# Performance work log

Measured on AMD Instinct MI355X. Metric: run time of the kernel, lower is better.

The kernel has to match this reference:

```python
import jax, jax.numpy as jnp
import numpy as np

B, DIN, D, T, C = 32768, 784, 256, 16, 64


def setup_inputs() -> dict:
    key = jax.random.key(0)
    ks = jax.random.split(key, 4)
    x = jax.random.normal(ks[0], (B, DIN), dtype=jnp.float32)
    Wp = jax.random.normal(ks[1], (DIN, D), dtype=jnp.float32) / np.sqrt(DIN).astype(np.float32)
    bp = jnp.zeros((D,), jnp.float32)
    sigs_raw = jax.random.normal(ks[2], (T, D), dtype=jnp.float32) * 0.5
    Wc = jax.random.normal(ks[3], (T, D, C), dtype=jnp.float32) / np.sqrt(D).astype(np.float32)
    bc = jnp.zeros((T, C), jnp.float32)
    return {"x": x, "Wp": Wp, "bp": bp, "sigs_raw": sigs_raw, "Wc": Wc, "bc": bc}


def _quantize_ternary(s):
    # straight-through ternary quantization with +/-0.3 thresholds
    q = jnp.where(s > 0.3, 1.0, jnp.where(s < -0.3, -1.0, 0.0)).astype(s.dtype)
    return s + jax.lax.stop_gradient(q - s)


def reference(x, Wp, bp, sigs_raw, Wc, bc):
    h = x @ Wp + bp                                   # [B, D]
    sigs = _quantize_ternary(sigs_raw)                # [T, D] ternary signatures
    scores = h @ sigs.T                               # [B, T]
    tile_indices = jnp.argmax(scores, axis=-1)        # [B] top-1 routing
    # per-tile linear classifiers, then select the routed tile's logits
    all_logits = jnp.einsum('bd,tdc->btc', h, Wc) + bc[None]   # [B, T, C]
    logits = jnp.take_along_axis(all_logits, tile_indices[:, None, None], axis=1)[:, 0, :]
    return logits, tile_indices
```

## Files before the change

kernel.cpp:

```cpp
#include <hip/hip_runtime.h>

typedef short short8 __attribute__((ext_vector_type(8)));
typedef float f32x4 __attribute__((ext_vector_type(4)));

#define B_ROWS 32768
#define DIN 784
#define D_DIM 256
#define T_TILES 16
#define C_DIM 64
#define BM 128
#define NCHUNK 25

#define WPT_OFF    0u
#define WCT_OFF    409600u
#define WS_OFF     933888u
#define BS_OFF     1034240u
#define H_OFF      1034368u
#define BUCKET_OFF 17811584u
#define CNT_OFF    19908736u

static __device__ inline unsigned short f2bf(float f) {
    unsigned u = __builtin_bit_cast(unsigned, f);
    u += 0x7fffu + ((u >> 16) & 1u);
    return (unsigned short)(u >> 16);
}
static __device__ inline double qtern(float s) {
    double v = (double)s;
    return (v > 0.3) ? 1.0 : ((v < -0.3) ? -1.0 : 0.0);
}

__global__ __launch_bounds__(256)
void prep_kernel(const float* __restrict__ Wp, const float* __restrict__ bp,
                 const float* __restrict__ sigs_raw, const float* __restrict__ Wc,
                 char* __restrict__ ws) {
    const int bid = blockIdx.x, tid = threadIdx.x;
    unsigned short* wpt = (unsigned short*)(ws + WPT_OFF);
    unsigned short* wct = (unsigned short*)(ws + WCT_OFF);
    double* Wsd = (double*)(ws + WS_OFF);
    double* bsd = (double*)(ws + BS_OFF);

    if (bid < 800) {
        const int k = bid;
        const float v = (k < DIN) ? Wp[(size_t)k * D_DIM + tid] : 0.f;
        wpt[(k >> 5) * 8192 + tid * 32 + (k & 31)] = f2bf(v);
    } else if (bid < 1584) {
        const int k = bid - 800;
        const int t = tid >> 4, l = tid & 15;
        double s = 0.0;
        for (int j = 0; j < 16; ++j) {
            const int d = l + 16 * j;
            s += (double)Wp[(size_t)k * D_DIM + d] * qtern(sigs_raw[t * D_DIM + d]);
        }
        #pragma unroll
        for (int m = 8; m >= 1; m >>= 1) s += __shfl_xor(s, m);
        if (l == 0) Wsd[k * 16 + t] = s;
    } else if (bid < 1600) {
        const int t = bid - 1584;
        const int c4 = (tid & 15) * 4, dg = (tid >> 4) * 16;
        for (int j = 0; j < 16; ++j) {
            const int d = dg + j;
            const float4 v = *(const float4*)&Wc[((size_t)t * D_DIM + d) * C_DIM + c4];
            wct[t * 16384 + (c4 + 0) * 256 + d] = f2bf(v.x);
            wct[t * 16384 + (c4 + 1) * 256 + d] = f2bf(v.y);
            wct[t * 16384 + (c4 + 2) * 256 + d] = f2bf(v.z);
            wct[t * 16384 + (c4 + 3) * 256 + d] = f2bf(v.w);
        }
    } else {
        if (tid < 16) {
            double s = 0.0;
            for (int d = 0; d < D_DIM; ++d)
                s += (double)bp[d] * qtern(sigs_raw[tid * D_DIM + d]);
            bsd[tid] = s;
        }
    }
}

__global__ __launch_bounds__(256, 2)
void gemm_score_kernel(const float* __restrict__ x, const float* __restrict__ bp,
                       char* __restrict__ ws, float* __restrict__ out) {
    __shared__ __align__(16) char u[61440];
    __shared__ int tidx_s[BM];

    unsigned short* Abuf = (unsigned short*)u;
    unsigned short* Bbuf = (unsigned short*)(u + 20480);
    const unsigned short* wpt = (const unsigned short*)(ws + WPT_OFF);
    unsigned short* hbf = (unsigned short*)(ws + H_OFF);
    const double* Wsd = (const double*)(ws + WS_OFF);
    const double* bsd = (const double*)(ws + BS_OFF);
    int* bucket = (int*)(ws + BUCKET_OFF);
    int* cnt = (int*)(ws + CNT_OFF);

    const int tid = threadIdx.x;
    const int row0 = blockIdx.x * BM;
    const int wid = tid >> 6, lane = tid & 63;
    const int wr = wid >> 1, wcid = wid & 1;
    const int lrow = lane & 15, kb8 = (lane >> 4) * 8;
    const int ar = tid >> 1, ako = (tid & 1) * 16;

    f32x4 acc[4][8];
    #pragma unroll
    for (int i = 0; i < 4; ++i)
        #pragma unroll
        for (int j = 0; j < 8; ++j) acc[i][j] = (f32x4){0.f, 0.f, 0.f, 0.f};

    float4 va[4], vb[4];
    {
        const bool valid = ako < DIN;
        const float4* p = (const float4*)&x[(size_t)(row0 + ar) * DIN + ako];
        va[0] = p[0]; va[1] = p[1]; va[2] = p[2]; va[3] = p[3];
        (void)valid;
        const float4* q = (const float4*)(wpt + 0 * 8192 + tid * 32);
        vb[0] = q[0]; vb[1] = q[1]; vb[2] = q[2]; vb[3] = q[3];
        unsigned short tmp[16];
        const float* f = (const float*)va;
        #pragma unroll
        for (int i = 0; i < 16; ++i) tmp[i] = f2bf(f[i]);
        unsigned short* da = Abuf + ar * 40 + ako;
        *(short8*)da = *(short8*)tmp; *(short8*)(da + 8) = *(short8*)(tmp + 8);
        unsigned short* db = Bbuf + tid * 40;
        *(float4*)db = vb[0]; *(float4*)(db + 8) = vb[1];
        *(float4*)(db + 16) = vb[2]; *(float4*)(db + 24) = vb[3];
    }
    __syncthreads();

    for (int c = 0; c < NCHUNK; ++c) {
        const int cur = c & 1;
        if (c + 1 < NCHUNK) {
            const int kbase = (c + 1) * 32 + ako;
            if (kbase < DIN) {
                const float4* p = (const float4*)&x[(size_t)(row0 + ar) * DIN + kbase];
                va[0] = p[0]; va[1] = p[1]; va[2] = p[2]; va[3] = p[3];
            } else {
                va[0] = va[1] = va[2] = va[3] = make_float4(0, 0, 0, 0);
            }
            const float4* q = (const float4*)(wpt + (c + 1) * 8192 + tid * 32);
            vb[0] = q[0]; vb[1] = q[1]; vb[2] = q[2]; vb[3] = q[3];
        }
        {
            const unsigned short* Ab = Abuf + cur * 5120;
            const unsigned short* Bb = Bbuf + cur * 10240;
            short8 af[4];
            #pragma unroll
            for (int rf = 0; rf < 4; ++rf)
                af[rf] = *(const short8*)(Ab + (wr * 64 + rf * 16 + lrow) * 40 + kb8);
            #pragma unroll
            for (int cf = 0; cf < 8; ++cf) {
                const short8 bfr = *(const short8*)(Bb + (wcid * 128 + cf * 16 + lrow) * 40 + kb8);
                #pragma unroll
                for (int rf = 0; rf < 4; ++rf)
                    acc[rf][cf] = __builtin_amdgcn_mfma_f32_16x16x32_bf16(af[rf], bfr, acc[rf][cf], 0, 0, 0);
            }
        }
        if (c + 1 < NCHUNK) {
            unsigned short tmp[16];
            const float* f = (const float*)va;
            #pragma unroll
            for (int i = 0; i < 16; ++i) tmp[i] = f2bf(f[i]);
            unsigned short* da = Abuf + (cur ^ 1) * 5120 + ar * 40 + ako;
            *(short8*)da = *(short8*)tmp; *(short8*)(da + 8) = *(short8*)(tmp + 8);
            unsigned short* db = Bbuf + (cur ^ 1) * 10240 + tid * 40;
            *(float4*)db = vb[0]; *(float4*)(db + 8) = vb[1];
            *(float4*)(db + 16) = vb[2]; *(float4*)(db + 24) = vb[3];
        }
        __syncthreads();
    }

    #pragma unroll
    for (int cf = 0; cf < 8; ++cf) {
        const int gc = wcid * 128 + cf * 16 + lrow;
        const float bpv = bp[gc];
        #pragma unroll
        for (int rf = 0; rf < 4; ++rf) {
            const int grow = row0 + wr * 64 + rf * 16 + (lane >> 4) * 4;
            #pragma unroll
            for (int r = 0; r < 4; ++r)
                hbf[(size_t)(grow + r) * D_DIM + gc] = f2bf(acc[rf][cf][r] + bpv);
        }
    }

    float*  xs  = (float*)u;
    double* wss = (double*)(u + 34816);
    double* scs = (double*)(u + 43008);

    const int sr = tid >> 1, stg = tid & 1, skh = (tid & 1) * 32;
    double accd[8];
    #pragma unroll
    for (int j = 0; j < 8; ++j) accd[j] = bsd[stg * 8 + j];

    for (int c = 0; c < 13; ++c) {
        __syncthreads();
        #pragma unroll
        for (int i = 0; i < 8; ++i) {
            const int k = c * 64 + skh + i * 4;
            float4 v = (k + 4 <= DIN) ? *(const float4*)&x[(size_t)(row0 + sr) * DIN + k]
                                      : make_float4(0, 0, 0, 0);
            *(float4*)&xs[sr * 68 + skh + i * 4] = v;
        }
        {
            const int k = tid >> 2, tq = (tid & 3) * 4;
            const int gk = c * 64 + k;
            double2 w0, w1;
            if (gk < DIN) {
                w0 = *(const double2*)&Wsd[gk * 16 + tq];
                w1 = *(const double2*)&Wsd[gk * 16 + tq + 2];
            } else { w0.x = w0.y = w1.x = w1.y = 0.0; }
            *(double2*)&wss[k * 16 + tq] = w0;
            *(double2*)&wss[k * 16 + tq + 2] = w1;
        }
        __syncthreads();
        #pragma unroll 4
        for (int k = 0; k < 64; ++k) {
            const double xv = (double)xs[sr * 68 + k];
            const double* wrow = &wss[k * 16 + stg * 8];
            #pragma unroll
            for (int j = 0; j < 8; ++j) accd[j] += xv * wrow[j];
        }
    }
    __syncthreads();
    #pragma unroll
    for (int j = 0; j < 8; ++j) scs[sr * 18 + stg * 8 + j] = accd[j];
    __syncthreads();

    if (tid < BM) {
        const double* s = &scs[tid * 18];
        double best = s[0]; int bi = 0;
        #pragma unroll
        for (int t = 1; t < 16; ++t)
            if (s[t] > best) { best = s[t]; bi = t; }
        tidx_s[tid] = bi;
        out[(size_t)B_ROWS * C_DIM + row0 + tid] = (float)bi;
    }
    __syncthreads();
    if (tid < T_TILES) {
        int c = 0;
        for (int r = 0; r < BM; ++r) c += (tidx_s[r] == tid);
        int pos = atomicAdd(&cnt[tid], c);
        for (int r = 0; r < BM; ++r)
            if (tidx_s[r] == tid) bucket[tid * B_ROWS + (pos++)] = row0 + r;
    }
}

__global__ __launch_bounds__(256)
void logits_kernel(const float* __restrict__ bc, const char* __restrict__ ws,
                   float* __restrict__ out) {
    __shared__ __align__(16) unsigned short As[128 * 72];
    __shared__ __align__(16) unsigned short Bs[64 * 72];
    __shared__ int rows_s[128];

    const int tid = threadIdx.x;
    const int t = blockIdx.x >> 8;
    const int c0 = (blockIdx.x & 255) * 128;
    const int* cnt = (const int*)(ws + CNT_OFF);
    const int cntv = cnt[t];
    if (c0 >= cntv) return;

    const int* bucket = (const int*)(ws + BUCKET_OFF);
    const unsigned short* hbf = (const unsigned short*)(ws + H_OFF);
    const unsigned short* wct = (const unsigned short*)(ws + WCT_OFF);

    if (tid < 128) {
        int i = c0 + tid; if (i >= cntv) i = cntv - 1;
        rows_s[tid] = bucket[t * B_ROWS + i];
    }
    __syncthreads();

    const int wid = tid >> 6, lane = tid & 63;
    const int wr = wid >> 1, wcid = wid & 1;
    const int lrow = lane & 15, kb8 = (lane >> 4) * 8;
    const int ar = tid >> 1, akh = (tid & 1) * 32;

    f32x4 acc[4][2];
    #pragma unroll
    for (int i = 0; i < 4; ++i) { acc[i][0] = (f32x4){0,0,0,0}; acc[i][1] = (f32x4){0,0,0,0}; }

    for (int ch = 0; ch < 4; ++ch) {
        {
            const float4* p = (const float4*)&hbf[(size_t)rows_s[ar] * D_DIM + ch * 64 + akh];
            const float4 v0 = p[0], v1 = p[1], v2 = p[2], v3 = p[3];
            unsigned short* dst = As + ar * 72 + akh;
            *(float4*)dst = v0; *(float4*)(dst + 8) = v1;
            *(float4*)(dst + 16) = v2; *(float4*)(dst + 24) = v3;
        }
        if (tid < 128) {
            const int cc = tid >> 1, ckh = (tid & 1) * 32;
            const float4* p = (const float4*)&wct[t * 16384 + cc * 256 + ch * 64 + ckh];
            const float4 v0 = p[0], v1 = p[1], v2 = p[2], v3 = p[3];
            unsigned short* dst = Bs + cc * 72 + ckh;
            *(float4*)dst = v0; *(float4*)(dst + 8) = v1;
            *(float4*)(dst + 16) = v2; *(float4*)(dst + 24) = v3;
        }
        __syncthreads();
        #pragma unroll
        for (int ks = 0; ks < 2; ++ks) {
            const int kb = ks * 32 + kb8;
            short8 bf0 = *(const short8*)(Bs + (wcid * 32 + 0 * 16 + lrow) * 72 + kb);
            short8 bf1 = *(const short8*)(Bs + (wcid * 32 + 1 * 16 + lrow) * 72 + kb);
            #pragma unroll
            for (int rf = 0; rf < 4; ++rf) {
                const short8 af = *(const short8*)(As + (wr * 64 + rf * 16 + lrow) * 72 + kb);
                acc[rf][0] = __builtin_amdgcn_mfma_f32_16x16x32_bf16(af, bf0, acc[rf][0], 0, 0, 0);
                acc[rf][1] = __builtin_amdgcn_mfma_f32_16x16x32_bf16(af, bf1, acc[rf][1], 0, 0, 0);
            }
        }
        __syncthreads();
    }

    #pragma unroll
    for (int cf = 0; cf < 2; ++cf) {
        const int col = wcid * 32 + cf * 16 + lrow;
        const float bcv = bc[t * C_DIM + col];
        #pragma unroll
        for (int rf = 0; rf < 4; ++rf) {
            const int lr = wr * 64 + rf * 16 + (lane >> 4) * 4;
            #pragma unroll
            for (int r = 0; r < 4; ++r)
                out[(size_t)rows_s[lr + r] * C_DIM + col] = acc[rf][cf][r] + bcv;
        }
    }
}

extern "C" void kernel_launch(void* const* d_in, const int* in_sizes, int n_in,
                              void* d_out, int out_size, void* d_ws, size_t ws_size,
                              hipStream_t stream) {
    const float* x    = (const float*)d_in[0];
    const float* Wp   = (const float*)d_in[1];
    const float* bp   = (const float*)d_in[2];
    const float* sigs = (const float*)d_in[3];
    const float* Wc   = (const float*)d_in[4];
    const float* bc   = (const float*)d_in[5];
    float* out = (float*)d_out;
    char* ws = (char*)d_ws;

    hipMemsetAsync(ws + CNT_OFF, 0, 64, stream);
    prep_kernel<<<dim3(1601), dim3(256), 0, stream>>>(Wp, bp, sigs, Wc, ws);
    gemm_score_kernel<<<dim3(B_ROWS / BM), dim3(256), 0, stream>>>(x, bp, ws, out);
    logits_kernel<<<dim3(16 * 256), dim3(256), 0, stream>>>(bc, ws, out);
}
```

Baseline: 283.4 us.

## Fuse fp64 routing score into GEMM main loop and shrink row tile

Result: faster. 235.8 us (-16.8%).

```diff
diff --git a/kernel.cpp b/kernel.cpp
--- a/kernel.cpp
+++ b/kernel.cpp
@@ -8,16 +8,16 @@
 #define D_DIM 256
 #define T_TILES 16
 #define C_DIM 64
-#define BM 128
+#define BM 64
 #define NCHUNK 25
 
 #define WPT_OFF    0u
 #define WCT_OFF    409600u
 #define WS_OFF     933888u
-#define BS_OFF     1034240u
-#define H_OFF      1034368u
-#define BUCKET_OFF 17811584u
-#define CNT_OFF    19908736u
+#define BS_OFF     1036288u
+#define H_OFF      1036416u
+#define BUCKET_OFF 17813632u
+#define CNT_OFF    19910784u
 
 static __device__ inline unsigned short f2bf(float f) {
     unsigned u = __builtin_bit_cast(unsigned, f);
@@ -33,56 +33,94 @@
 void prep_kernel(const float* __restrict__ Wp, const float* __restrict__ bp,
                  const float* __restrict__ sigs_raw, const float* __restrict__ Wc,
                  char* __restrict__ ws) {
+    __shared__ __align__(16) char u2[34816];
     const int bid = blockIdx.x, tid = threadIdx.x;
     unsigned short* wpt = (unsigned short*)(ws + WPT_OFF);
     unsigned short* wct = (unsigned short*)(ws + WCT_OFF);
     double* Wsd = (double*)(ws + WS_OFF);
     double* bsd = (double*)(ws + BS_OFF);
 
-    if (bid < 800) {
-        const int k = bid;
-        const float v = (k < DIN) ? Wp[(size_t)k * D_DIM + tid] : 0.f;
-        wpt[(k >> 5) * 8192 + tid * 32 + (k & 31)] = f2bf(v);
-    } else if (bid < 1584) {
-        const int k = bid - 800;
+    if (bid < 25) {
+        unsigned short (*lt)[40] = (unsigned short (*)[40])u2;
+        const int k0 = bid * 32;
+        #pragma unroll
+        for (int p = 0; p < 8; ++p) {
+            const int k = p * 4 + (tid >> 6);
+            const int c = (tid & 63) * 4;
+            float4 v = make_float4(0.f, 0.f, 0.f, 0.f);
+            if (k0 + k < DIN) v = *(const float4*)&Wp[(size_t)(k0 + k) * D_DIM + c];
+            lt[c + 0][k] = f2bf(v.x); lt[c + 1][k] = f2bf(v.y);
+            lt[c + 2][k] = f2bf(v.z); lt[c + 3][k] = f2bf(v.w);
+        }
+        __syncthreads();
+        const float4* src = (const float4*)&lt[tid][0];
+        float4* dst = (float4*)(wpt + bid * 8192 + tid * 32);
+        dst[0] = src[0]; dst[1] = src[1]; dst[2] = src[2]; dst[3] = src[3];
+    } else if (bid < 123) {
+        float* sigq = (float*)u2;
+        float* wp8  = (float*)(u2 + 16384);
+        const int k0 = (bid - 25) * 8;
+        #pragma unroll
+        for (int i = 0; i < 16; ++i) {
+            const int idx = i * 256 + tid;
+            sigq[idx] = (float)qtern(sigs_raw[idx]);
+        }
+        #pragma unroll
+        for (int i = 0; i < 8; ++i)
+            wp8[i * 256 + tid] = Wp[(size_t)(k0 + i) * D_DIM + tid];
+        __syncthreads();
+        const int kk = tid >> 5, t = (tid >> 1) & 15, half = tid & 1;
+        double s = 0.0;
+        const float* wr = &wp8[kk * 256 + half * 128];
+        const float* sq = &sigq[t * 256 + half * 128];
+        for (int d = 0; d < 128; ++d) s += (double)wr[d] * (double)sq[d];
+        s += __shfl_xor(s, 1);
+        if (half == 0) Wsd[(k0 + kk) * 16 + t] = s;
+    } else if (bid < 139) {
+        unsigned short (*lc)[264] = (unsigned short (*)[264])u2;
+        const int t = bid - 123;
+        #pragma unroll
+        for (int j = 0; j < 16; ++j) {
+            const int f4 = j * 256 + tid;
+            const int d  = f4 >> 4;
+            const int c4 = (f4 & 15) * 4;
+            const float4 v = *(const float4*)&Wc[((size_t)t * D_DIM + d) * C_DIM + c4];
+            lc[c4 + 0][d] = f2bf(v.x); lc[c4 + 1][d] = f2bf(v.y);
+            lc[c4 + 2][d] = f2bf(v.z); lc[c4 + 3][d] = f2bf(v.w);
+        }
+        __syncthreads();
+        const int c = tid >> 2, d0 = (tid & 3) * 64;
+        const float4* src = (const float4*)&lc[c][d0];
+        float4* dst = (float4*)(wct + t * 16384 + c * 256 + d0);
+        #pragma unroll
+        for (int i = 0; i < 8; ++i) dst[i] = src[i];
+    } else {
+        int* cnt = (int*)(ws + CNT_OFF);
+        if (tid < 16) cnt[tid] = 0;
+        Wsd[12544 + tid] = 0.0;
         const int t = tid >> 4, l = tid & 15;
         double s = 0.0;
+        #pragma unroll
         for (int j = 0; j < 16; ++j) {
-            const int d = l + 16 * j;
-            s += (double)Wp[(size_t)k * D_DIM + d] * qtern(sigs_raw[t * D_DIM + d]);
+            const int d = l * 16 + j;
+            s += (double)bp[d] * qtern(sigs_raw[t * D_DIM + d]);
         }
         #pragma unroll
         for (int m = 8; m >= 1; m >>= 1) s += __shfl_xor(s, m);
-        if (l == 0) Wsd[k * 16 + t] = s;
-    } else if (bid < 1600) {
-        const int t = bid - 1584;
-        const int c4 = (tid & 15) * 4, dg = (tid >> 4) * 16;
-        for (int j = 0; j < 16; ++j) {
-            const int d = dg + j;
-            const float4 v = *(const float4*)&Wc[((size_t)t * D_DIM + d) * C_DIM + c4];
-            wct[t * 16384 + (c4 + 0) * 256 + d] = f2bf(v.x);
-            wct[t * 16384 + (c4 + 1) * 256 + d] = f2bf(v.y);
-            wct[t * 16384 + (c4 + 2) * 256 + d] = f2bf(v.z);
-            wct[t * 16384 + (c4 + 3) * 256 + d] = f2bf(v.w);
-        }
-    } else {
-        if (tid < 16) {
-            double s = 0.0;
-            for (int d = 0; d < D_DIM; ++d)
-                s += (double)bp[d] * qtern(sigs_raw[tid * D_DIM + d]);
-            bsd[tid] = s;
-        }
+        if (l == 0) bsd[t] = s;
     }
 }
 
 __global__ __launch_bounds__(256, 2)
 void gemm_score_kernel(const float* __restrict__ x, const float* __restrict__ bp,
                        char* __restrict__ ws, float* __restrict__ out) {
-    __shared__ __align__(16) char u[61440];
+    __shared__ __align__(16) char u[59904];
     __shared__ int tidx_s[BM];
 
     unsigned short* Abuf = (unsigned short*)u;
-    unsigned short* Bbuf = (unsigned short*)(u + 20480);
+    unsigned short* Bbuf = (unsigned short*)(u + 10240);
+    double*         wss  = (double*)(u + 51200);
+
     const unsigned short* wpt = (const unsigned short*)(ws + WPT_OFF);
     unsigned short* hbf = (unsigned short*)(ws + H_OFF);
     const double* Wsd = (const double*)(ws + WS_OFF);
@@ -95,142 +133,133 @@
     const int wid = tid >> 6, lane = tid & 63;
     const int wr = wid >> 1, wcid = wid & 1;
     const int lrow = lane & 15, kb8 = (lane >> 4) * 8;
-    const int ar = tid >> 1, ako = (tid & 1) * 16;
-
-    f32x4 acc[4][8];
-    #pragma unroll
-    for (int i = 0; i < 4; ++i)
+    const int ar = tid >> 2, ako = (tid & 3) * 8;
+    const int wk = tid >> 3, wt = (tid * 2) & 15;
+
+    f32x4 acc[2][8];
+    #pragma unroll
+    for (int i = 0; i < 2; ++i)
         #pragma unroll
         for (int j = 0; j < 8; ++j) acc[i][j] = (f32x4){0.f, 0.f, 0.f, 0.f};
-
-    float4 va[4], vb[4];
+    double accd[16];
+    #pragma unroll
+    for (int t = 0; t < 16; ++t) accd[t] = 0.0;
+    float xs8[8];
+
     {
-        const bool valid = ako < DIN;
         const float4* p = (const float4*)&x[(size_t)(row0 + ar) * DIN + ako];
-        va[0] = p[0]; va[1] = p[1]; va[2] = p[2]; va[3] = p[3];
-        (void)valid;
-        const float4* q = (const float4*)(wpt + 0 * 8192 + tid * 32);
-        vb[0] = q[0]; vb[1] = q[1]; vb[2] = q[2]; vb[3] = q[3];
-        unsigned short tmp[16];
-        const float* f = (const float*)va;
-        #pragma unroll
-        for (int i = 0; i < 16; ++i) tmp[i] = f2bf(f[i]);
-        unsigned short* da = Abuf + ar * 40 + ako;
-        *(short8*)da = *(short8*)tmp; *(short8*)(da + 8) = *(short8*)(tmp + 8);
-        unsigned short* db = Bbuf + tid * 40;
-        *(float4*)db = vb[0]; *(float4*)(db + 8) = vb[1];
-        *(float4*)(db + 16) = vb[2]; *(float4*)(db + 24) = vb[3];
+        const float4 a0 = p[0], a1 = p[1];
+        xs8[0] = a0.x; xs8[1] = a0.y; xs8[2] = a0.z; xs8[3] = a0.w;
+        xs8[4] = a1.x; xs8[5] = a1.y; xs8[6] = a1.z; xs8[7] = a1.w;
+        unsigned short tmp[8];
+        #pragma unroll
+        for (int i = 0; i < 8; ++i) tmp[i] = f2bf(xs8[i]);
+        *(short8*)(Abuf + ar * 40 + ako) = *(short8*)tmp;
+        const float4* q = (const float4*)(wpt + tid * 32);
+        float4* db = (float4*)(Bbuf + tid * 40);
+        db[0] = q[0]; db[1] = q[1]; db[2] = q[2]; db[3] = q[3];
+        const double w0 = Wsd[tid * 2], w1 = Wsd[tid * 2 + 1];
+        wss[wk * 17 + wt] = w0; wss[wk * 17 + wt + 1] = w1;
     }
     __syncthreads();
 
     for (int c = 0; c < NCHUNK; ++c) {
         const int cur = c & 1;
-        if (c + 1 < NCHUNK) {
+        const bool more = (c + 1 < NCHUNK);
+        float4 va0, va1, vb0, vb1, vb2, vb3;
+        double w0 = 0.0, w1 = 0.0;
+        if (more) {
             const int kbase = (c + 1) * 32 + ako;
             if (kbase < DIN) {
                 const float4* p = (const float4*)&x[(size_t)(row0 + ar) * DIN + kbase];
-                va[0] = p[0]; va[1] = p[1]; va[2] = p[2]; va[3] = p[3];
+                va0 = p[0]; va1 = p[1];
             } else {
-                va[0] = va[1] = va[2] = va[3] = make_float4(0, 0, 0, 0);
+                va0 = make_float4(0, 0, 0, 0); va1 = make_float4(0, 0, 0, 0);
             }
             const float4* q = (const float4*)(wpt + (c + 1) * 8192 + tid * 32);
-            vb[0] = q[0]; vb[1] = q[1]; vb[2] = q[2]; vb[3] = q[3];
+            vb0 = q[0]; vb1 = q[1]; vb2 = q[2]; vb3 = q[3];
+            w0 = Wsd[(c + 1) * 512 + tid * 2];
+            w1 = Wsd[(c + 1) * 512 + tid * 2 + 1];
         }
         {
-            const unsigned short* Ab = Abuf + cur * 5120;
+            const unsigned short* Ab = Abuf + cur * 2560;
             const unsigned short* Bb = Bbuf + cur * 10240;
-            short8 af[4];
-            #pragma unroll
-            for (int rf = 0; rf < 4; ++rf)
-                af[rf] = *(const short8*)(Ab + (wr * 64 + rf * 16 + lrow) * 40 + kb8);
+            const short8 af0 = *(const short8*)(Ab + (wr * 32 + lrow) * 40 + kb8);
+            const short8 af1 = *(const short8*)(Ab + (wr * 32 + 16 + lrow) * 40 + kb8);
             #pragma unroll
             for (int cf = 0; cf < 8; ++cf) {
                 const short8 bfr = *(const short8*)(Bb + (wcid * 128 + cf * 16 + lrow) * 40 + kb8);
+                acc[0][cf] = __builtin_amdgcn_mfma_f32_16x16x32_bf16(af0, bfr, acc[0][cf], 0, 0, 0);
+                acc[1][cf] = __builtin_amdgcn_mfma_f32_16x16x32_bf16(af1, bfr, acc[1][cf], 0, 0, 0);
+            }
+        }
+        {
+            const double* wbase = wss + cur * 544;
+            #pragma unroll
+            for (int i = 0; i < 8; ++i) {
+                const double xv = (double)xs8[i];
+                const double* wrow = wbase + (ako + i) * 17;
                 #pragma unroll
-                for (int rf = 0; rf < 4; ++rf)
-                    acc[rf][cf] = __builtin_amdgcn_mfma_f32_16x16x32_bf16(af[rf], bfr, acc[rf][cf], 0, 0, 0);
+                for (int t = 0; t < 16; ++t) accd[t] += xv * wrow[t];
             }
         }
-        if (c + 1 < NCHUNK) {
-            unsigned short tmp[16];
-            const float* f = (const float*)va;
-            #pragma unroll
-            for (int i = 0; i < 16; ++i) tmp[i] = f2bf(f[i]);
-            unsigned short* da = Abuf + (cur ^ 1) * 5120 + ar * 40 + ako;
-            *(short8*)da = *(short8*)tmp; *(short8*)(da + 8) = *(short8*)(tmp + 8);
-            unsigned short* db = Bbuf + (cur ^ 1) * 10240 + tid * 40;
-            *(float4*)db = vb[0]; *(float4*)(db + 8) = vb[1];
-            *(float4*)(db + 16) = vb[2]; *(float4*)(db + 24) = vb[3];
-        }
-        __syncthreads();
-    }
-
+        if (more) {
+            xs8[0] = va0.x; xs8[1] = va0.y; xs8[2] = va0.z; xs8[3] = va0.w;
+            xs8[4] = va1.x; xs8[5] = va1.y; xs8[6] = va1.z; xs8[7] = va1.w;
+            unsigned short tmp[8];
+            #pragma unroll
+            for (int i = 0; i < 8; ++i) tmp[i] = f2bf(xs8[i]);
+            *(short8*)(Abuf + (cur ^ 1) * 2560 + ar * 40 + ako) = *(short8*)tmp;
+            float4* db = (float4*)(Bbuf + (cur ^ 1) * 10240 + tid * 40);
+            db[0] = vb0; db[1] = vb1; db[2] = vb2; db[3] = vb3;
+            wss[(cur ^ 1) * 544 + wk * 17 + wt] = w0;
+            wss[(cur ^ 1) * 544 + wk * 17 + wt + 1] = w1;
+        }
+        __syncthreads();
+    }
+
+    unsigned short* h_s = (unsigned short*)u;
     #pragma unroll
     for (int cf = 0; cf < 8; ++cf) {
         const int gc = wcid * 128 + cf * 16 + lrow;
         const float bpv = bp[gc];
         #pragma unroll
-        for (int rf = 0; rf < 4; ++rf) {
-            const int grow = row0 + wr * 64 + rf * 16 + (lane >> 4) * 4;
+        for (int rf = 0; rf < 2; ++rf) {
+            const int lr = wr * 32 + rf * 16 + (lane >> 4) * 4;
             #pragma unroll
             for (int r = 0; r < 4; ++r)
-                hbf[(size_t)(grow + r) * D_DIM + gc] = f2bf(acc[rf][cf][r] + bpv);
-        }
-    }
-
-    float*  xs  = (float*)u;
-    double* wss = (double*)(u + 34816);
-    double* scs = (double*)(u + 43008);
-
-    const int sr = tid >> 1, stg = tid & 1, skh = (tid & 1) * 32;
-    double accd[8];
-    #pragma unroll
-    for (int j = 0; j < 8; ++j) accd[j] = bsd[stg * 8 + j];
-
-    for (int c = 0; c < 13; ++c) {
-        __syncthreads();
-        #pragma unroll
-        for (int i = 0; i < 8; ++i) {
-            const int k = c * 64 + skh + i * 4;
-            float4 v = (k + 4 <= DIN) ? *(const float4*)&x[(size_t)(row0 + sr) * DIN + k]
-                                      : make_float4(0, 0, 0, 0);
-            *(float4*)&xs[sr * 68 + skh + i * 4] = v;
-        }
-        {
-            const int k = tid >> 2, tq = (tid & 3) * 4;
-            const int gk = c * 64 + k;
-            double2 w0, w1;
-            if (gk < DIN) {
-                w0 = *(const double2*)&Wsd[gk * 16 + tq];
-                w1 = *(const double2*)&Wsd[gk * 16 + tq + 2];
-            } else { w0.x = w0.y = w1.x = w1.y = 0.0; }
-            *(double2*)&wss[k * 16 + tq] = w0;
-            *(double2*)&wss[k * 16 + tq + 2] = w1;
-        }
-        __syncthreads();
-        #pragma unroll 4
-        for (int k = 0; k < 64; ++k) {
-            const double xv = (double)xs[sr * 68 + k];
-            const double* wrow = &wss[k * 16 + stg * 8];
-            #pragma unroll
-            for (int j = 0; j < 8; ++j) accd[j] += xv * wrow[j];
-        }
+                h_s[(lr + r) * 264 + gc] = f2bf(acc[rf][cf][r] + bpv);
+        }
+    }
+
+    #pragma unroll
+    for (int t = 0; t < 16; ++t) {
+        accd[t] += __shfl_xor(accd[t], 1);
+        accd[t] += __shfl_xor(accd[t], 2);
+    }
+    if ((tid & 3) == 0) {
+        double best = -1.0e300; int bi = 0;
+        #pragma unroll
+        for (int t = 0; t < 16; ++t) {
+            const double v = accd[t] + bsd[t];
+            if (v > best) { best = v; bi = t; }
+        }
+        tidx_s[ar] = bi;
+        out[(size_t)B_ROWS * C_DIM + row0 + ar] = (float)bi;
     }
     __syncthreads();
-    #pragma unroll
-    for (int j = 0; j < 8; ++j) scs[sr * 18 + stg * 8 + j] = accd[j];
-    __syncthreads();
-
-    if (tid < BM) {
-        const double* s = &scs[tid * 18];
-        double best = s[0]; int bi = 0;
-        #pragma unroll
-        for (int t = 1; t < 16; ++t)
-            if (s[t] > best) { best = s[t]; bi = t; }
-        tidx_s[tid] = bi;
-        out[(size_t)B_ROWS * C_DIM + row0 + tid] = (float)bi;
-    }
-    __syncthreads();
+
+    {
+        const int r = tid >> 2, q = tid & 3;
+        const float4* src = (const float4*)(h_s + r * 264 + q * 64);
+        float4 v[8];
+        #pragma unroll
+        for (int i = 0; i < 8; ++i) v[i] = src[i];
+        float4* dst = (float4*)(hbf + (size_t)(row0 + r) * D_DIM + q * 64);
+        #pragma unroll
+        for (int i = 0; i < 8; ++i) dst[i] = v[i];
+    }
+
     if (tid < T_TILES) {
         int c = 0;
         for (int r = 0; r < BM; ++r) c += (tidx_s[r] == tid);
@@ -243,8 +272,8 @@
 __global__ __launch_bounds__(256)
 void logits_kernel(const float* __restrict__ bc, const char* __restrict__ ws,
                    float* __restrict__ out) {
-    __shared__ __align__(16) unsigned short As[128 * 72];
-    __shared__ __align__(16) unsigned short Bs[64 * 72];
+    __shared__ __align__(16) unsigned short As[128 * 136];
+    __shared__ __align__(16) unsigned short Bs[64 * 136];
     __shared__ int rows_s[128];
 
     const int tid = threadIdx.x;
@@ -267,37 +296,43 @@
     const int wid = tid >> 6, lane = tid & 63;
     const int wr = wid >> 1, wcid = wid & 1;
     const int lrow = lane & 15, kb8 = (lane >> 4) * 8;
-    const int ar = tid >> 1, akh = (tid & 1) * 32;
 
     f32x4 acc[4][2];
     #pragma unroll
     for (int i = 0; i < 4; ++i) { acc[i][0] = (f32x4){0,0,0,0}; acc[i][1] = (f32x4){0,0,0,0}; }
 
-    for (int ch = 0; ch < 4; ++ch) {
+    #pragma unroll
+    for (int ch = 0; ch < 2; ++ch) {
+        const int k0 = ch * 128;
         {
-            const float4* p = (const float4*)&hbf[(size_t)rows_s[ar] * D_DIM + ch * 64 + akh];
-            const float4 v0 = p[0], v1 = p[1], v2 = p[2], v3 = p[3];
-            unsigned short* dst = As + ar * 72 + akh;
-            *(float4*)dst = v0; *(float4*)(dst + 8) = v1;
-            *(float4*)(dst + 16) = v2; *(float4*)(dst + 24) = v3;
+            const int r = tid >> 1, h64 = (tid & 1) * 64;
+            const float4* p = (const float4*)(hbf + (size_t)rows_s[r] * D_DIM + k0 + h64);
+            float4 v[8];
+            #pragma unroll
+            for (int i = 0; i < 8; ++i) v[i] = p[i];
+            float4* d = (float4*)(As + r * 136 + h64);
+            #pragma unroll
+            for (int i = 0; i < 8; ++i) d[i] = v[i];
         }
         if (tid < 128) {
-            const int cc = tid >> 1, ckh = (tid & 1) * 32;
-            const float4* p = (const float4*)&wct[t * 16384 + cc * 256 + ch * 64 + ckh];
-            const float4 v0 = p[0], v1 = p[1], v2 = p[2], v3 = p[3];
-            unsigned short* dst = Bs + cc * 72 + ckh;
-            *(float4*)dst = v0; *(float4*)(dst + 8) = v1;
-            *(float4*)(dst + 16) = v2; *(float4*)(dst + 24) = v3;
-        }
-        __syncthreads();
-        #pragma unroll
-        for (int ks = 0; ks < 2; ++ks) {
+            const int c = tid >> 1, h64 = (tid & 1) * 64;
+            const float4* p = (const float4*)(wct + (size_t)t * 16384 + c * 256 + k0 + h64);
+            float4 v[8];
+            #pragma unroll
+            for (int i = 0; i < 8; ++i) v[i] = p[i];
+            float4* d = (float4*)(Bs + c * 136 + h64);
+            #pragma unroll
+            for (int i = 0; i < 8; ++i) d[i] = v[i];
+        }
+        __syncthreads();
+        #pragma unroll
+        for (int ks = 0; ks < 4; ++ks) {
             const int kb = ks * 32 + kb8;
-            short8 bf0 = *(const short8*)(Bs + (wcid * 32 + 0 * 16 + lrow) * 72 + kb);
-            short8 bf1 = *(const short8*)(Bs + (wcid * 32 + 1 * 16 + lrow) * 72 + kb);
+            const short8 bf0 = *(const short8*)(Bs + (wcid * 32 + lrow) * 136 + kb);
+            const short8 bf1 = *(const short8*)(Bs + (wcid * 32 + 16 + lrow) * 136 + kb);
             #pragma unroll
             for (int rf = 0; rf < 4; ++rf) {
-                const short8 af = *(const short8*)(As + (wr * 64 + rf * 16 + lrow) * 72 + kb);
+                const short8 af = *(const short8*)(As + (wr * 64 + rf * 16 + lrow) * 136 + kb);
                 acc[rf][0] = __builtin_amdgcn_mfma_f32_16x16x32_bf16(af, bf0, acc[rf][0], 0, 0, 0);
                 acc[rf][1] = __builtin_amdgcn_mfma_f32_16x16x32_bf16(af, bf1, acc[rf][1], 0, 0, 0);
             }
@@ -331,8 +366,7 @@
     float* out = (float*)d_out;
     char* ws = (char*)d_ws;
 
-    hipMemsetAsync(ws + CNT_OFF, 0, 64, stream);
-    prep_kernel<<<dim3(1601), dim3(256), 0, stream>>>(Wp, bp, sigs, Wc, ws);
+    prep_kernel<<<dim3(140), dim3(256), 0, stream>>>(Wp, bp, sigs, Wc, ws);
     gemm_score_kernel<<<dim3(B_ROWS / BM), dim3(256), 0, stream>>>(x, bp, ws, out);
     logits_kernel<<<dim3(16 * 256), dim3(256), 0, stream>>>(bc, ws, out);
 }
```
